# Kernel optimization log

Measured on AMD Instinct MI355X. Metric: run time of the kernel, lower is better.

The kernel has to match this reference:

```python
import jax, jax.numpy as jnp
import numpy as np

B, C, D = 16, 1024, 512
H = 8
E, K = 8, 2
FF = 4 * D
CAP_FACTOR = 1.25
T = B * C
CAP = int(CAP_FACTOR * T * K / E)  # 5120
EPS = 1e-5


def setup_inputs() -> dict:
    key = jax.random.key(0)
    ks = jax.random.split(key, 16)
    s = 0.02
    return {
        "x": jax.random.normal(ks[0], (B, C, D), jnp.float32),
        "src_mask": jnp.ones((B, 1, 1, C), jnp.int32),
        "wq": jax.random.normal(ks[1], (D, D), jnp.float32) * s,
        "bq": jnp.zeros((D,), jnp.float32),
        "wk": jax.random.normal(ks[2], (D, D), jnp.float32) * s,
        "bk": jnp.zeros((D,), jnp.float32),
        "wv": jax.random.normal(ks[3], (D, D), jnp.float32) * s,
        "bv": jnp.zeros((D,), jnp.float32),
        "wo": jax.random.normal(ks[4], (D, D), jnp.float32) * s,
        "bo": jnp.zeros((D,), jnp.float32),
        "ln1_g": jnp.ones((D,), jnp.float32),
        "ln1_b": jnp.zeros((D,), jnp.float32),
        "ln2_g": jnp.ones((D,), jnp.float32),
        "ln2_b": jnp.zeros((D,), jnp.float32),
        "router_w": jax.random.normal(ks[5], (D, E), jnp.float32) * s,
        "w1": jax.random.normal(ks[6], (E, D, FF), jnp.float32) * s,
        "b1": jnp.zeros((E, FF), jnp.float32),
        "w2": jax.random.normal(ks[7], (E, FF, D), jnp.float32) * s,
        "b2": jnp.zeros((E, D), jnp.float32),
    }


def _layernorm(z, g, b):
    m = z.mean(-1, keepdims=True)
    v = jnp.mean((z - m) ** 2, -1, keepdims=True)
    return (z - m) * jax.lax.rsqrt(v + EPS) * g + b


def _attention(x, mask, wq, bq, wk, bk, wv, bv, wo, bo):
    hd = D // H
    q = (x @ wq + bq).reshape(B, C, H, hd).transpose(0, 2, 1, 3)  # bhqd
    k = (x @ wk + bk).reshape(B, C, H, hd).transpose(0, 2, 1, 3)
    v = (x @ wv + bv).reshape(B, C, H, hd).transpose(0, 2, 1, 3)
    scores = jnp.einsum("bhqd,bhkd->bhqk", q, k) * (1.0 / np.sqrt(hd))
    scores = jnp.where(mask == 0, jnp.float32(-1e10), scores)
    attn = jax.nn.softmax(scores, axis=-1)
    o = jnp.einsum("bhqk,bhkd->bhqd", attn, v)
    o = o.transpose(0, 2, 1, 3).reshape(B, C, D)
    return o @ wo + bo


def _sparse_moe(x, router_w, w1, b1, w2, b2):
    xf = x.reshape(T, D)
    probs = jax.nn.softmax(xf @ router_w, axis=-1)  # [T, E]
    topv, topi = jax.lax.top_k(probs, K)            # [T, K]
    topv = topv / topv.sum(-1, keepdims=True)
    fe = topi.reshape(T * K)                        # expert id per slot
    oh = jax.nn.one_hot(fe, E, dtype=jnp.int32)     # [T*K, E]
    pos = (jnp.cumsum(oh, axis=0) * oh).sum(-1) - 1 # rank within expert
    keep = pos < CAP
    pos_safe = jnp.where(keep, pos, CAP)            # CAP -> dropped via mode='drop'
    tok = jnp.repeat(jnp.arange(T), K)
    disp = jnp.zeros((E, CAP, D), xf.dtype).at[fe, pos_safe].set(
        xf[tok], mode="drop")                       # [E, CAP, D]
    h = jax.nn.gelu(jnp.einsum("ecd,edf->ecf", disp, w1) + b1[:, None, :])
    y = jnp.einsum("ecf,efd->ecd", h, w2) + b2[:, None, :]
    gathered = y[fe, jnp.minimum(pos_safe, CAP - 1)]      # [T*K, D]
    gathered = jnp.where(keep[:, None], gathered, 0.0)
    out = (gathered.reshape(T, K, D) * topv[:, :, None]).sum(1)
    return out.reshape(B, C, D)


def reference(x, src_mask, wq, bq, wk, bk, wv, bv, wo, bo,
              ln1_g, ln1_b, ln2_g, ln2_b, router_w, w1, b1, w2, b2):
    attn_out = _attention(x, src_mask, wq, bq, wk, bk, wv, bv, wo, bo)
    src = _layernorm(x + attn_out, ln1_g, ln1_b)
    ff = _sparse_moe(src, router_w, w1, b1, w2, b2)
    return _layernorm(src + ff, ln2_g, ln2_b)
```

## Files before the change

### kernel.cpp

```cpp
#include <hip/hip_runtime.h>


#define DEV __device__ __forceinline__

typedef __bf16 bf16x8 __attribute__((ext_vector_type(8)));
typedef float  f32x4  __attribute__((ext_vector_type(4)));

typedef __attribute__((address_space(1))) unsigned char uchar_g;
typedef __attribute__((address_space(3))) unsigned char uchar_l;

DEV unsigned short f2bf(float f){
  __bf16 b = (__bf16)f;
  return __builtin_bit_cast(unsigned short, b);
}
DEV float bf2f(unsigned short h){
  return __builtin_bit_cast(float, ((unsigned)h) << 16);
}
DEV float geluf(float z){
  float a = 0.7978845608028654f*(z + 0.044715f*z*z*z);
  a = fminf(fmaxf(a, -15.f), 15.f);
  float u = __expf(-2.f*a);
  float th = (1.f - u) / (1.f + u);
  return 0.5f*z*(1.f + th);
}

template<int LOGROWB, int NBYTES>
DEV void stage_tile(char* lds, const char* g0, long stride, int tid){
  #pragma unroll
  for (int it = 0; it < NBYTES/4096; ++it){
    int o   = tid*16 + it*4096;
    int row = o >> LOGROWB;
    int b0  = o & ((1 << LOGROWB) - 1);
    int swz = (row & ((1 << (LOGROWB-4)) - 1)) << 4;
    const char* src = g0 + (long)row*stride + (b0 ^ swz);
    char* lb = lds + ((tid >> 6) << 10) + (it << 12);
    __builtin_amdgcn_global_load_lds((uchar_g*)src, (uchar_l*)lb, 16, 0, 0);
  }
}

DEV void stage_gather(char* lds, const char* base, const int* rowTok, int k0b, int tid){
  #pragma unroll
  for (int it = 0; it < 2; ++it){
    int o   = tid*16 + it*4096;
    int row = o >> 6;
    int b0  = o & 63;
    int swz = (row & 3) << 4;
    const char* src = base + (long)rowTok[row]*1024 + k0b + (b0 ^ swz);
    char* lb = lds + ((tid >> 6) << 10) + (it << 12);
    __builtin_amdgcn_global_load_lds((uchar_g*)src, (uchar_l*)lb, 16, 0, 0);
  }
}

template<int LOGROWB>
DEV bf16x8 frag(const char* lds, int row, int kByte){
  int swz = (row & ((1 << (LOGROWB-4)) - 1)) << 4;
  const char* p = lds + ((long)row << LOGROWB) + (kByte ^ swz);
  bf16x8 v;
  __builtin_memcpy(&v, __builtin_assume_aligned(p, 16), 16);
  return v;
}

DEV f32x4 mfma16(bf16x8 a, bf16x8 b, f32x4 c){
  return __builtin_amdgcn_mfma_f32_16x16x32_bf16(a, b, c, 0, 0, 0);
}

DEV float wsum64(float v){
  #pragma unroll
  for (int off = 32; off; off >>= 1) v += __shfl_xor(v, off);
  return v;
}
DEV float wsum16(float v){
  v += __shfl_xor(v, 1); v += __shfl_xor(v, 2);
  v += __shfl_xor(v, 4); v += __shfl_xor(v, 8);
  return v;
}
DEV float wmax16(float v){
  v = fmaxf(v, __shfl_xor(v, 1)); v = fmaxf(v, __shfl_xor(v, 2));
  v = fmaxf(v, __shfl_xor(v, 4)); v = fmaxf(v, __shfl_xor(v, 8));
  return v;
}


__global__ __launch_bounds__(256) void split_x_k(const float* __restrict__ x,
    unsigned short* __restrict__ xh, unsigned short* __restrict__ xl, int n4)
{
  int i = blockIdx.x*256 + threadIdx.x;
  if (i >= n4) return;
  float4 v = ((const float4*)x)[i];
  ushort4 h, lo;
  h.x = f2bf(v.x); lo.x = f2bf(v.x - bf2f(h.x));
  h.y = f2bf(v.y); lo.y = f2bf(v.y - bf2f(h.y));
  h.z = f2bf(v.z); lo.z = f2bf(v.z - bf2f(h.z));
  h.w = f2bf(v.w); lo.w = f2bf(v.w - bf2f(h.w));
  ((ushort4*)xh)[i] = h;
  ((ushort4*)xl)[i] = lo;
}

__global__ __launch_bounds__(256) void convT_k(const float* __restrict__ in,
    unsigned short* __restrict__ outh, unsigned short* __restrict__ outl,
    int K, int N, int rowOff)
{
  __shared__ float t[32][33];
  long zin  = (long)blockIdx.z * K * N;
  long zout = (long)blockIdx.z * N * K;
  int n0 = blockIdx.x*32, k0 = blockIdx.y*32;
  int cid = threadIdx.x & 31, rid = threadIdx.x >> 5;
  #pragma unroll
  for (int j = 0; j < 4; ++j){
    int r = rid + j*8;
    t[r][cid] = in[zin + (long)(k0+r)*N + n0 + cid];
  }
  __syncthreads();
  #pragma unroll
  for (int j = 0; j < 4; ++j){
    int nr = rid + j*8;
    float v = t[cid][nr];
    long o = zout + (long)(rowOff + n0 + nr)*K + k0 + cid;
    unsigned short hb = f2bf(v);
    outh[o] = hb;
    if (outl) outl[o] = f2bf(v - bf2f(hb));
  }
}

__global__ __launch_bounds__(256) void vtrans_k(const unsigned short* __restrict__ vin,
    unsigned short* __restrict__ vout)
{
  __shared__ unsigned short t[64][65];
  int bh = blockIdx.y, c0 = blockIdx.x*64;
  const unsigned short* src = vin + ((long)bh*1024 + c0)*64;
  for (int j = threadIdx.x; j < 4096; j += 256){
    int r = j >> 6, c = j & 63;
    t[r][c] = src[r*64 + c];
  }
  __syncthreads();
  unsigned short* dst = vout + (long)bh*64*1024 + c0;
  for (int j = threadIdx.x; j < 4096; j += 256){
    int d = j >> 6, cc = j & 63;
    dst[(long)d*1024 + cc] = t[cc][d];
  }
}


#define GEMM_PRE \
  const int tid = threadIdx.x, w = tid>>6, l = tid&63; \
  const int wm = (w>>1)*64, wn = (w&1)*64; \
  f32x4 acc[4][4] = {};

#define GEMM3_INNER(SAH,SAL,SBH,SBL) do { \
  const int kb = (l>>4)<<4; \
  bf16x8 ah_[4], al_[4], bh_[4], bl_[4]; \
  _Pragma("unroll") \
  for (int mt=0; mt<4; ++mt){ int r = wm+mt*16+(l&15); ah_[mt]=frag<6>(SAH,r,kb); al_[mt]=frag<6>(SAL,r,kb); } \
  _Pragma("unroll") \
  for (int nt=0; nt<4; ++nt){ int r = wn+nt*16+(l&15); bh_[nt]=frag<6>(SBH,r,kb); bl_[nt]=frag<6>(SBL,r,kb); } \
  _Pragma("unroll") \
  for (int mt=0; mt<4; ++mt) \
    _Pragma("unroll") \
    for (int nt=0; nt<4; ++nt){ \
      acc[mt][nt] = mfma16(ah_[mt], bh_[nt], acc[mt][nt]); \
      acc[mt][nt] = mfma16(ah_[mt], bl_[nt], acc[mt][nt]); \
      acc[mt][nt] = mfma16(al_[mt], bh_[nt], acc[mt][nt]); \
    } \
} while(0)

#define GEMM1_INNER(SA,SB) do { \
  const int kb = (l>>4)<<4; \
  bf16x8 a_[4], b_[4]; \
  _Pragma("unroll") \
  for (int mt=0; mt<4; ++mt){ a_[mt]=frag<6>(SA, wm+mt*16+(l&15), kb); } \
  _Pragma("unroll") \
  for (int nt=0; nt<4; ++nt){ b_[nt]=frag<6>(SB, wn+nt*16+(l&15), kb); } \
  _Pragma("unroll") \
  for (int mt=0; mt<4; ++mt) \
    _Pragma("unroll") \
    for (int nt=0; nt<4; ++nt) acc[mt][nt] = mfma16(a_[mt], b_[nt], acc[mt][nt]); \
} while(0)

__global__ __launch_bounds__(256) void gemm_qkv(
    const char* __restrict__ ah, const char* __restrict__ al,
    const char* __restrict__ bh, const char* __restrict__ bl,
    const float* __restrict__ bq, const float* __restrict__ bk, const float* __restrict__ bv,
    unsigned short* __restrict__ qh, unsigned short* __restrict__ ql,
    unsigned short* __restrict__ kh, unsigned short* __restrict__ kl,
    unsigned short* __restrict__ vh, unsigned short* __restrict__ vl)
{
  __shared__ __align__(16) char sAh[8192], sAl[8192], sBh[8192], sBl[8192];
  const int m0 = blockIdx.x*128, n0 = blockIdx.y*128;
  GEMM_PRE
  for (int k0 = 0; k0 < 512; k0 += 32){
    __syncthreads();
    stage_tile<6,8192>(sAh, ah + (long)m0*1024 + k0*2, 1024, tid);
    stage_tile<6,8192>(sAl, al + (long)m0*1024 + k0*2, 1024, tid);
    stage_tile<6,8192>(sBh, bh + (long)n0*1024 + k0*2, 1024, tid);
    stage_tile<6,8192>(sBl, bl + (long)n0*1024 + k0*2, 1024, tid);
    __syncthreads();
    GEMM3_INNER(sAh, sAl, sBh, sBl);
  }
  #pragma unroll
  for (int nt = 0; nt < 4; ++nt){
    int col = n0 + wn + nt*16 + (l&15);
    int mat = col >> 9;
    int dcol = col & 511;
    float bias = (mat==0) ? bq[dcol] : (mat==1) ? bk[dcol] : bv[dcol];
    unsigned short* dh = (mat==0) ? qh : (mat==1) ? kh : vh;
    unsigned short* dl = (mat==0) ? ql : (mat==1) ? kl : vl;
    int hh = dcol >> 6, dd = dcol & 63;
    #pragma unroll
    for (int mt = 0; mt < 4; ++mt)
      #pragma unroll
      for (int i = 0; i < 4; ++i){
        int rowg = m0 + wm + mt*16 + (l>>4)*4 + i;
        int b_ = rowg >> 10, c_ = rowg & 1023;
        long o = ((long)(b_*8 + hh)*1024 + c_)*64 + dd;
        float v = acc[mt][nt][i] + bias;
        unsigned short hb = f2bf(v);
        dh[o] = hb;
        dl[o] = f2bf(v - bf2f(hb));
      }
  }
}

__global__ __launch_bounds__(256) void gemm_oproj(
    const char* __restrict__ ah, const char* __restrict__ al,
    const char* __restrict__ bh, const char* __restrict__ bl,
    const float* __restrict__ bo, float* __restrict__ outp)
{
  __shared__ __align__(16) char sAh[8192], sAl[8192], sBh[8192], sBl[8192];
  const int m0 = blockIdx.x*128, n0 = blockIdx.y*128;
  GEMM_PRE
  for (int k0 = 0; k0 < 512; k0 += 32){
    __syncthreads();
    stage_tile<6,8192>(sAh, ah + (long)m0*1024 + k0*2, 1024, tid);
    stage_tile<6,8192>(sAl, al + (long)m0*1024 + k0*2, 1024, tid);
    stage_tile<6,8192>(sBh, bh + (long)n0*1024 + k0*2, 1024, tid);
    stage_tile<6,8192>(sBl, bl + (long)n0*1024 + k0*2, 1024, tid);
    __syncthreads();
    GEMM3_INNER(sAh, sAl, sBh, sBl);
  }
  #pragma unroll
  for (int nt = 0; nt < 4; ++nt){
    int col = n0 + wn + nt*16 + (l&15);
    float bias = bo[col];
    #pragma unroll
    for (int mt = 0; mt < 4; ++mt)
      #pragma unroll
      for (int i = 0; i < 4; ++i){
        int rowg = m0 + wm + mt*16 + (l>>4)*4 + i;
        outp[(long)rowg*512 + col] = acc[mt][nt][i] + bias;
      }
  }
}

__global__ __launch_bounds__(256) void gemm_ffn1(
    const char* __restrict__ srcb, const int* __restrict__ idx, const int* __restrict__ cntc,
    const char* __restrict__ w1T, const float* __restrict__ b1,
    unsigned short* __restrict__ hbuf, int ffc, int rr)
{
  const int e = blockIdx.z;
  const int m0 = blockIdx.x*128;
  if (m0 >= cntc[e]) return;
  const int n0 = blockIdx.y*128;
  const int ffg0 = rr*ffc;
  __shared__ __align__(16) char sA[8192], sB[8192];
  GEMM_PRE
  for (int k0 = 0; k0 < 512; k0 += 32){
    __syncthreads();
    stage_gather(sA, srcb, idx + e*5120 + m0, k0*2, tid);
    stage_tile<6,8192>(sB, w1T + ((long)e*2048 + ffg0 + n0)*1024 + k0*2, 1024, tid);
    __syncthreads();
    GEMM1_INNER(sA, sB);
  }
  #pragma unroll
  for (int nt = 0; nt < 4; ++nt){
    int colc = n0 + wn + nt*16 + (l&15);
    float bias = b1[e*2048 + ffg0 + colc];
    #pragma unroll
    for (int mt = 0; mt < 4; ++mt)
      #pragma unroll
      for (int i = 0; i < 4; ++i){
        int rowg = m0 + wm + mt*16 + (l>>4)*4 + i;
        float v = geluf(acc[mt][nt][i] + bias);
        hbuf[((long)e*5120 + rowg)*ffc + colc] = f2bf(v);
      }
  }
}

__global__ __launch_bounds__(256) void gemm_ffn2(
    const unsigned short* __restrict__ hbuf, const int* __restrict__ cntc,
    const char* __restrict__ w2T, const float* __restrict__ b2,
    float* __restrict__ y, int ffc, int rr)
{
  const int e = blockIdx.z;
  const int m0 = blockIdx.x*128;
  if (m0 >= cntc[e]) return;
  const int n0 = blockIdx.y*128;
  __shared__ __align__(16) char sA[8192], sB[8192];
  GEMM_PRE
  for (int k0 = 0; k0 < ffc; k0 += 32){
    __syncthreads();
    stage_tile<6,8192>(sA, (const char*)hbuf + ((long)e*5120 + m0)*(ffc*2) + k0*2, ffc*2, tid);
    stage_tile<6,8192>(sB, w2T + ((long)e*512 + n0)*4096 + (rr*ffc + k0)*2, 4096, tid);
    __syncthreads();
    GEMM1_INNER(sA, sB);
  }
  #pragma unroll
  for (int nt = 0; nt < 4; ++nt){
    int col = n0 + wn + nt*16 + (l&15);
    #pragma unroll
    for (int mt = 0; mt < 4; ++mt)
      #pragma unroll
      for (int i = 0; i < 4; ++i){
        int rowg = m0 + wm + mt*16 + (l>>4)*4 + i;
        long o = ((long)e*5120 + rowg)*512 + col;
        float base = (rr == 0) ? b2[e*512 + col] : y[o];
        y[o] = base + acc[mt][nt][i];
      }
  }
}

__global__ __launch_bounds__(256) void flash_attn(
    const char* __restrict__ qh, const char* __restrict__ ql,
    const char* __restrict__ kh, const char* __restrict__ kl,
    const char* __restrict__ vth, const char* __restrict__ vtl,
    const int* __restrict__ msk,
    unsigned short* __restrict__ oh, unsigned short* __restrict__ ol)
{
  __shared__ __align__(16) char lds[49152];
  char* sKh = lds;
  char* sKl = lds + 8192;
  char* sVh = lds + 16384;
  char* sVl = lds + 24576;
  const int tid = threadIdx.x, w = tid>>6, l = tid&63;
  const int q0 = blockIdx.x*64;
  const int bh = blockIdx.y, b_ = bh>>3, h_ = bh&7;
  char* pw = lds + 32768 + w*4096;

  stage_tile<7,8192>(lds,        qh + ((long)bh*1024 + q0)*128, 128, tid);
  stage_tile<7,8192>(lds + 8192, ql + ((long)bh*1024 + q0)*128, 128, tid);
  __syncthreads();
  bf16x8 qfh[2], qfl[2];
  const int ra = w*16 + (l&15);
  #pragma unroll
  for (int ks = 0; ks < 2; ++ks){
    const int kb = ks*64 + ((l>>4)<<4);
    qfh[ks] = frag<7>(lds,        ra, kb);
    qfl[ks] = frag<7>(lds + 8192, ra, kb);
  }

  float mrow[4], lrow[4];
  f32x4 oacc[4] = {};
  #pragma unroll
  for (int i = 0; i < 4; ++i){ mrow[i] = -1e30f; lrow[i] = 0.0f; }
  const int* mb = msk + b_*1024;

  for (int kv0 = 0; kv0 < 1024; kv0 += 64){
    __syncthreads();
    stage_tile<7,8192>(sKh, kh + ((long)bh*1024 + kv0)*128, 128, tid);
    stage_tile<7,8192>(sKl, kl + ((long)bh*1024 + kv0)*128, 128, tid);
    stage_tile<7,8192>(sVh, vth + (long)bh*131072 + kv0*2, 2048, tid);
    stage_tile<7,8192>(sVl, vtl + (long)bh*131072 + kv0*2, 2048, tid);
    __syncthreads();

    f32x4 sacc[4] = {};
    __builtin_amdgcn_s_setprio(1);
    #pragma unroll
    for (int ks = 0; ks < 2; ++ks){
      const int kb = ks*64 + ((l>>4)<<4);
      #pragma unroll
      for (int nt = 0; nt < 4; ++nt){
        const int rb = nt*16 + (l&15);
        bf16x8 b_h = frag<7>(sKh, rb, kb);
        bf16x8 b_l = frag<7>(sKl, rb, kb);
        sacc[nt] = mfma16(qfh[ks], b_h, sacc[nt]);
        sacc[nt] = mfma16(qfh[ks], b_l, sacc[nt]);
        sacc[nt] = mfma16(qfl[ks], b_h, sacc[nt]);
      }
    }
    __builtin_amdgcn_s_setprio(0);

    float sv[4][4];
    #pragma unroll
    for (int nt = 0; nt < 4; ++nt){
      int mk = mb[kv0 + nt*16 + (l&15)];
      #pragma unroll
      for (int i = 0; i < 4; ++i){
        float s = sacc[nt][i] * 0.125f;
        sv[nt][i] = (mk == 0) ? -1e10f : s;
      }
    }
    float tmax[4]; bool need = false;
    #pragma unroll
    for (int i = 0; i < 4; ++i){
      float tm = fmaxf(fmaxf(sv[0][i], sv[1][i]), fmaxf(sv[2][i], sv[3][i]));
      tmax[i] = wmax16(tm);
      need |= (tmax[i] > mrow[i] + 8.0f);
    }
    if (__ballot(need) != 0ull){
      #pragma unroll
      for (int i = 0; i < 4; ++i){
        float mn  = fmaxf(mrow[i], tmax[i]);
        float fsc = __expf(mrow[i] - mn);
        lrow[i] *= fsc; mrow[i] = mn;
        #pragma unroll
        for (int dt = 0; dt < 4; ++dt) oacc[dt][i] *= fsc;
      }
    }
    float tsum[4] = {0,0,0,0};
    float pf[4][4];
    #pragma unroll
    for (int nt = 0; nt < 4; ++nt)
      #pragma unroll
      for (int i = 0; i < 4; ++i){
        float p = __expf(sv[nt][i] - mrow[i]);
        pf[nt][i] = p; tsum[i] += p;
      }
    #pragma unroll
    for (int i = 0; i < 4; ++i) lrow[i] += wsum16(tsum[i]);

    #pragma unroll
    for (int nt = 0; nt < 4; ++nt)
      #pragma unroll
      for (int i = 0; i < 4; ++i){
        int r = (l>>4)*4 + i;
        int cbyte = (nt*16 + (l&15))*2;
        int off = r*128 + (cbyte ^ ((r&7)<<4));
        unsigned short hb = f2bf(pf[nt][i]);
        *(unsigned short*)(pw + off)        = hb;
        *(unsigned short*)(pw + 2048 + off) = f2bf(pf[nt][i] - bf2f(hb));
      }
    __builtin_amdgcn_s_setprio(1);
    #pragma unroll
    for (int ks = 0; ks < 2; ++ks){
      const int kb = ks*64 + ((l>>4)<<4);
      bf16x8 p_h = frag<7>(pw,        l&15, kb);
      bf16x8 p_l = frag<7>(pw + 2048, l&15, kb);
      #pragma unroll
      for (int dt = 0; dt < 4; ++dt){
        const int rv = dt*16 + (l&15);
        bf16x8 v_h = frag<7>(sVh, rv, kb);
        bf16x8 v_l = frag<7>(sVl, rv, kb);
        oacc[dt] = mfma16(p_h, v_h, oacc[dt]);
        oacc[dt] = mfma16(p_h, v_l, oacc[dt]);
        oacc[dt] = mfma16(p_l, v_h, oacc[dt]);
      }
    }
    __builtin_amdgcn_s_setprio(0);
  }
  #pragma unroll
  for (int dt = 0; dt < 4; ++dt)
    #pragma unroll
    for (int i = 0; i < 4; ++i){
      float val = oacc[dt][i] / lrow[i];
      int qg = q0 + w*16 + (l>>4)*4 + i;
      long o = ((long)(b_*1024 + qg))*512 + h_*64 + dt*16 + (l&15);
      unsigned short hb = f2bf(val);
      oh[o] = hb;
      ol[o] = f2bf(val - bf2f(hb));
    }
}


__global__ __launch_bounds__(256) void ln1_k(const float* __restrict__ x,
    const float* __restrict__ attn, const float* __restrict__ g, const float* __restrict__ bb,
    float* __restrict__ src, unsigned short* __restrict__ srcb)
{
  const int w = threadIdx.x >> 6, l = threadIdx.x & 63;
  const long t = (long)blockIdx.x*4 + w;
  const float* xr = x + t*512;
  const float* ar = attn + t*512;
  float z[8]; float s = 0.f;
  #pragma unroll
  for (int j = 0; j < 8; ++j){ int d = l + j*64; z[j] = xr[d] + ar[d]; s += z[j]; }
  s = wsum64(s);
  float mean = s * (1.f/512.f);
  float vs = 0.f;
  #pragma unroll
  for (int j = 0; j < 8; ++j){ float d = z[j]-mean; vs += d*d; }
  vs = wsum64(vs);
  float rstd = 1.f / sqrtf(vs*(1.f/512.f) + 1e-5f);
  #pragma unroll
  for (int j = 0; j < 8; ++j){
    int d = l + j*64;
    float o = (z[j]-mean)*rstd*g[d] + bb[d];
    src[t*512 + d] = o;
    srcb[t*512 + d] = f2bf(o);
  }
}

__global__ __launch_bounds__(256) void router_k(const float* __restrict__ src,
    const float* __restrict__ rw, int* __restrict__ topi, float* __restrict__ topv)
{
  const int w = threadIdx.x >> 6, l = threadIdx.x & 63;
  const long t = (long)blockIdx.x*4 + w;
  const float* xr = src + t*512;
  float acc[8] = {0,0,0,0,0,0,0,0};
  #pragma unroll
  for (int j = 0; j < 8; ++j){
    int d = l + j*64;
    float xv = xr[d];
    #pragma unroll
    for (int e = 0; e < 8; ++e) acc[e] += xv * rw[d*8 + e];
  }
  #pragma unroll
  for (int e = 0; e < 8; ++e) acc[e] = wsum64(acc[e]);
  int i1 = 0; float v1 = acc[0];
  #pragma unroll
  for (int e = 1; e < 8; ++e){ if (acc[e] > v1){ v1 = acc[e]; i1 = e; } }
  int i2 = -1; float v2 = -1e30f;
  #pragma unroll
  for (int e = 0; e < 8; ++e){ if (e != i1 && acc[e] > v2){ v2 = acc[e]; i2 = e; } }
  if (l == 0){
    topi[2*t]   = i1;
    topi[2*t+1] = i2;
    topv[2*t]   = 1.0f / (1.0f + __expf(v2 - v1));
    topv[2*t+1] = 1.0f / (1.0f + __expf(v1 - v2));
  }
}

__global__ __launch_bounds__(1024) void rank_k(const int* __restrict__ topi,
    int* __restrict__ pos, int* __restrict__ idx, int* __restrict__ cntc)
{
  __shared__ int hist[1024][8];
  const int t = threadIdx.x;
  for (int j = t; j < 8*5120; j += 1024) idx[j] = 0;
  int c[8] = {0,0,0,0,0,0,0,0};
  const int base = t*32;
  for (int j = 0; j < 32; ++j){
    int e = topi[base + j];
    #pragma unroll
    for (int e2 = 0; e2 < 8; ++e2) c[e2] += (e == e2);
  }
  #pragma unroll
  for (int e2 = 0; e2 < 8; ++e2) hist[t][e2] = c[e2];
  __syncthreads();
  const int wv = t >> 6, l = t & 63;
  if (wv < 8){
    int vals[16]; int s = 0;
    #pragma unroll
    for (int j = 0; j < 16; ++j){ vals[j] = hist[l*16 + j][wv]; s += vals[j]; }
    int sc = s;
    #pragma unroll
    for (int off = 1; off < 64; off <<= 1){
      int n = __shfl_up(sc, off);
      if (l >= off) sc += n;
    }
    int run = sc - s;
    #pragma unroll
    for (int j = 0; j < 16; ++j){ int v = vals[j]; hist[l*16 + j][wv] = run; run += v; }
    if (l == 63) cntc[wv] = (run < 5120) ? run : 5120;
  }
  __syncthreads();
  int r2[8];
  #pragma unroll
  for (int e2 = 0; e2 < 8; ++e2) r2[e2] = hist[t][e2];
  for (int j = 0; j < 32; ++j){
    int slot = base + j;
    int e = topi[slot];
    int p = 0;
    #pragma unroll
    for (int e2 = 0; e2 < 8; ++e2){ int m = (e == e2); p += m ? r2[e2] : 0; r2[e2] += m; }
    pos[slot] = p;
    if (p < 5120) idx[e*5120 + p] = slot >> 1;
  }
}

__global__ __launch_bounds__(256) void final_k(const float* __restrict__ src,
    const float* __restrict__ y, const int* __restrict__ topi,
    const float* __restrict__ topv, const int* __restrict__ pos,
    const float* __restrict__ g, const float* __restrict__ bb,
    float* __restrict__ out)
{
  const int w = threadIdx.x >> 6, l = threadIdx.x & 63;
  const long t = (long)blockIdx.x*4 + w;
  const int e0 = topi[2*t], e1 = topi[2*t+1];
  const int p0 = pos[2*t],  p1 = pos[2*t+1];
  const float w0 = topv[2*t], w1 = topv[2*t+1];
  const bool k0 = (p0 < 5120), k1 = (p1 < 5120);
  const float* y0 = y + ((long)e0*5120 + (k0 ? p0 : 0))*512;
  const float* y1 = y + ((long)e1*5120 + (k1 ? p1 : 0))*512;
  const float* sr = src + t*512;
  float z[8]; float s = 0.f;
  #pragma unroll
  for (int j = 0; j < 8; ++j){
    int d = l + j*64;
    float f0 = k0 ? y0[d] : 0.f;
    float f1 = k1 ? y1[d] : 0.f;
    z[j] = sr[d] + w0*f0 + w1*f1;
    s += z[j];
  }
  s = wsum64(s);
  float mean = s * (1.f/512.f);
  float vs = 0.f;
  #pragma unroll
  for (int j = 0; j < 8; ++j){ float d = z[j]-mean; vs += d*d; }
  vs = wsum64(vs);
  float rstd = 1.f / sqrtf(vs*(1.f/512.f) + 1e-5f);
  #pragma unroll
  for (int j = 0; j < 8; ++j){
    int d = l + j*64;
    out[t*512 + d] = (z[j]-mean)*rstd*g[d] + bb[d];
  }
}


extern "C" void kernel_launch(void* const* d_in, const int* in_sizes, int n_in,
                              void* d_out, int out_size, void* d_ws, size_t ws_size,
                              hipStream_t stream)
{
  const float* x   = (const float*)d_in[0];
  const int*   msk = (const int*)  d_in[1];
  const float* wq  = (const float*)d_in[2];
  const float* bq  = (const float*)d_in[3];
  const float* wk  = (const float*)d_in[4];
  const float* bk  = (const float*)d_in[5];
  const float* wv  = (const float*)d_in[6];
  const float* bv  = (const float*)d_in[7];
  const float* wo  = (const float*)d_in[8];
  const float* bo  = (const float*)d_in[9];
  const float* g1  = (const float*)d_in[10];
  const float* be1 = (const float*)d_in[11];
  const float* g2  = (const float*)d_in[12];
  const float* be2 = (const float*)d_in[13];
  const float* rw  = (const float*)d_in[14];
  const float* w1  = (const float*)d_in[15];
  const float* b1  = (const float*)d_in[16];
  const float* w2  = (const float*)d_in[17];
  const float* b2  = (const float*)d_in[18];
  float* out = (float*)d_out;
  char* ws = (char*)d_ws;

  const long SZ = 16777216;
  char* xh = ws;             char* xl = ws + SZ;
  char* oh = xh;             char* ol = xl;
  char* qh = ws + 2*SZ;      char* ql = ws + 3*SZ;
  float* oproj = (float*)(ws + 2*SZ);
  char* vth = ws + 4*SZ;     char* vtl = ws + 5*SZ;
  float* ybuf = (float*)ws;
  char* kh = ws + 6*SZ;      char* kl = ws + 7*SZ;
  float* srcf = (float*)(ws + 6*SZ);
  char* vh = ws + 8*SZ;      char* vl = ws + 9*SZ;
  char* srcb = ws + 8*SZ;
  int*   topi  = (int*)  (ws + 9*SZ);
  float* topv  = (float*)(ws + 9*SZ + 131072);
  int*   pos   = (int*)  (ws + 9*SZ + 262144);
  int*   idx   = (int*)  (ws + 9*SZ + 393216);
  int*   cntc  = (int*)  (ws + 9*SZ + 557056);
  char* wqkvTh = ws + 10*SZ;
  char* wqkvTl = wqkvTh + 1572864;
  char* woTh   = wqkvTl + 1572864;
  char* woTl   = woTh + 524288;
  char* w1T    = woTl + 524288;
  char* w2T    = w1T + SZ;
  char* hbuf   = w2T + SZ;

  int R = 8;
  {
    size_t base = (size_t)(hbuf - ws);
    const int cand[4] = {1, 2, 4, 8};
    for (int i = 0; i < 4; ++i){
      size_t need = base + (size_t)167772160 / (size_t)cand[i];
      if (need <= ws_size){ R = cand[i]; break; }
    }
  }
  const int FFC = 2048 / R;

  split_x_k<<<8192,256,0,stream>>>(x, (unsigned short*)xh, (unsigned short*)xl, 2097152);
  convT_k<<<dim3(16,16,1),256,0,stream>>>(wq, (unsigned short*)wqkvTh, (unsigned short*)wqkvTl, 512, 512, 0);
  convT_k<<<dim3(16,16,1),256,0,stream>>>(wk, (unsigned short*)wqkvTh, (unsigned short*)wqkvTl, 512, 512, 512);
  convT_k<<<dim3(16,16,1),256,0,stream>>>(wv, (unsigned short*)wqkvTh, (unsigned short*)wqkvTl, 512, 512, 1024);
  convT_k<<<dim3(16,16,1),256,0,stream>>>(wo, (unsigned short*)woTh, (unsigned short*)woTl, 512, 512, 0);
  convT_k<<<dim3(64,16,8),256,0,stream>>>(w1, (unsigned short*)w1T, nullptr, 512, 2048, 0);
  convT_k<<<dim3(16,64,8),256,0,stream>>>(w2, (unsigned short*)w2T, nullptr, 2048, 512, 0);

  gemm_qkv<<<dim3(128,12),256,0,stream>>>(xh, xl, wqkvTh, wqkvTl, bq, bk, bv,
      (unsigned short*)qh, (unsigned short*)ql, (unsigned short*)kh, (unsigned short*)kl,
      (unsigned short*)vh, (unsigned short*)vl);
  vtrans_k<<<dim3(16,128),256,0,stream>>>((const unsigned short*)vh, (unsigned short*)vth);
  vtrans_k<<<dim3(16,128),256,0,stream>>>((const unsigned short*)vl, (unsigned short*)vtl);
  flash_attn<<<dim3(16,128),256,0,stream>>>(qh, ql, kh, kl, vth, vtl, msk,
      (unsigned short*)oh, (unsigned short*)ol);
  gemm_oproj<<<dim3(128,4),256,0,stream>>>(oh, ol, woTh, woTl, bo, oproj);
  ln1_k<<<4096,256,0,stream>>>(x, oproj, g1, be1, srcf, (unsigned short*)srcb);

  router_k<<<4096,256,0,stream>>>(srcf, rw, topi, topv);
  rank_k<<<1,1024,0,stream>>>(topi, pos, idx, cntc);

  for (int rr = 0; rr < R; ++rr){
    gemm_ffn1<<<dim3(40, FFC/128, 8),256,0,stream>>>(srcb, idx, cntc, w1T, b1,
        (unsigned short*)hbuf, FFC, rr);
    gemm_ffn2<<<dim3(40, 4, 8),256,0,stream>>>((const unsigned short*)hbuf, cntc, w2T, b2,
        ybuf, FFC, rr);
  }

  final_k<<<4096,256,0,stream>>>(srcf, ybuf, topi, topv, pos, g2, be2, out);
}
```

Baseline: 928.2 us.

## Chunk MoE FFN by expert groups instead of FF slices; fuse LN1 with router

The MoE FFN loop is now split over groups of experts instead of slices of the hidden FF dimension. Each ffn2 launch therefore runs the full K=2048 reduction and writes y once with the bias, instead of reading y back and accumulating across rounds. LayerNorm1 and the router are merged into one kernel so the normalized activations are not written and then read again. Flash attention now multiplies by a reciprocal of the row sum instead of dividing. The cost is fewer blocks per launch when R>1, which may lower occupancy.

Result: faster. 843.5 us (-9.1%).

```diff
diff --git a/kernel.cpp b/kernel.cpp
--- a/kernel.cpp
+++ b/kernel.cpp
@@ -254,66 +254,67 @@
 __global__ __launch_bounds__(256) void gemm_ffn1(
     const char* __restrict__ srcb, const int* __restrict__ idx, const int* __restrict__ cntc,
     const char* __restrict__ w1T, const float* __restrict__ b1,
-    unsigned short* __restrict__ hbuf, int ffc, int rr)
-{
-  const int e = blockIdx.z;
-  const int m0 = blockIdx.x*128;
-  if (m0 >= cntc[e]) return;
-  const int n0 = blockIdx.y*128;
-  const int ffg0 = rr*ffc;
-  __shared__ __align__(16) char sA[8192], sB[8192];
-  GEMM_PRE
-  for (int k0 = 0; k0 < 512; k0 += 32){
-    __syncthreads();
-    stage_gather(sA, srcb, idx + e*5120 + m0, k0*2, tid);
-    stage_tile<6,8192>(sB, w1T + ((long)e*2048 + ffg0 + n0)*1024 + k0*2, 1024, tid);
-    __syncthreads();
-    GEMM1_INNER(sA, sB);
-  }
-  #pragma unroll
-  for (int nt = 0; nt < 4; ++nt){
-    int colc = n0 + wn + nt*16 + (l&15);
-    float bias = b1[e*2048 + ffg0 + colc];
-    #pragma unroll
-    for (int mt = 0; mt < 4; ++mt)
-      #pragma unroll
-      for (int i = 0; i < 4; ++i){
-        int rowg = m0 + wm + mt*16 + (l>>4)*4 + i;
-        float v = geluf(acc[mt][nt][i] + bias);
-        hbuf[((long)e*5120 + rowg)*ffc + colc] = f2bf(v);
-      }
-  }
-}
-
-__global__ __launch_bounds__(256) void gemm_ffn2(
-    const unsigned short* __restrict__ hbuf, const int* __restrict__ cntc,
-    const char* __restrict__ w2T, const float* __restrict__ b2,
-    float* __restrict__ y, int ffc, int rr)
-{
-  const int e = blockIdx.z;
+    unsigned short* __restrict__ hbuf, int eg0)
+{
+  const int zl = blockIdx.z;
+  const int e = eg0 + zl;
   const int m0 = blockIdx.x*128;
   if (m0 >= cntc[e]) return;
   const int n0 = blockIdx.y*128;
   __shared__ __align__(16) char sA[8192], sB[8192];
   GEMM_PRE
-  for (int k0 = 0; k0 < ffc; k0 += 32){
-    __syncthreads();
-    stage_tile<6,8192>(sA, (const char*)hbuf + ((long)e*5120 + m0)*(ffc*2) + k0*2, ffc*2, tid);
-    stage_tile<6,8192>(sB, w2T + ((long)e*512 + n0)*4096 + (rr*ffc + k0)*2, 4096, tid);
+  for (int k0 = 0; k0 < 512; k0 += 32){
+    __syncthreads();
+    stage_gather(sA, srcb, idx + e*5120 + m0, k0*2, tid);
+    stage_tile<6,8192>(sB, w1T + ((long)e*2048 + n0)*1024 + k0*2, 1024, tid);
+    __syncthreads();
+    GEMM1_INNER(sA, sB);
+  }
+  #pragma unroll
+  for (int nt = 0; nt < 4; ++nt){
+    int colc = n0 + wn + nt*16 + (l&15);
+    float bias = b1[e*2048 + colc];
+    #pragma unroll
+    for (int mt = 0; mt < 4; ++mt)
+      #pragma unroll
+      for (int i = 0; i < 4; ++i){
+        int rowg = m0 + wm + mt*16 + (l>>4)*4 + i;
+        float v = geluf(acc[mt][nt][i] + bias);
+        hbuf[((long)zl*5120 + rowg)*2048 + colc] = f2bf(v);
+      }
+  }
+}
+
+__global__ __launch_bounds__(256) void gemm_ffn2(
+    const unsigned short* __restrict__ hbuf, const int* __restrict__ cntc,
+    const char* __restrict__ w2T, const float* __restrict__ b2,
+    float* __restrict__ y, int eg0)
+{
+  const int zl = blockIdx.z;
+  const int e = eg0 + zl;
+  const int m0 = blockIdx.x*128;
+  if (m0 >= cntc[e]) return;
+  const int n0 = blockIdx.y*128;
+  __shared__ __align__(16) char sA[8192], sB[8192];
+  GEMM_PRE
+  for (int k0 = 0; k0 < 2048; k0 += 32){
+    __syncthreads();
+    stage_tile<6,8192>(sA, (const char*)hbuf + ((long)zl*5120 + m0)*4096 + k0*2, 4096, tid);
+    stage_tile<6,8192>(sB, w2T + ((long)e*512 + n0)*4096 + k0*2, 4096, tid);
     __syncthreads();
     GEMM1_INNER(sA, sB);
   }
   #pragma unroll
   for (int nt = 0; nt < 4; ++nt){
     int col = n0 + wn + nt*16 + (l&15);
+    float bias = b2[e*512 + col];
     #pragma unroll
     for (int mt = 0; mt < 4; ++mt)
       #pragma unroll
       for (int i = 0; i < 4; ++i){
         int rowg = m0 + wm + mt*16 + (l>>4)*4 + i;
         long o = ((long)e*5120 + rowg)*512 + col;
-        float base = (rr == 0) ? b2[e*512 + col] : y[o];
-        y[o] = base + acc[mt][nt][i];
+        y[o] = bias + acc[mt][nt][i];
       }
   }
 }
@@ -446,11 +447,14 @@
     }
     __builtin_amdgcn_s_setprio(0);
   }
+  float rli[4];
+  #pragma unroll
+  for (int i = 0; i < 4; ++i) rli[i] = 1.0f / lrow[i];
   #pragma unroll
   for (int dt = 0; dt < 4; ++dt)
     #pragma unroll
     for (int i = 0; i < 4; ++i){
-      float val = oacc[dt][i] / lrow[i];
+      float val = oacc[dt][i] * rli[i];
       int qg = q0 + w*16 + (l>>4)*4 + i;
       long o = ((long)(b_*1024 + qg))*512 + h_*64 + dt*16 + (l&15);
       unsigned short hb = f2bf(val);
@@ -460,9 +464,11 @@
 }
 
 
-__global__ __launch_bounds__(256) void ln1_k(const float* __restrict__ x,
+__global__ __launch_bounds__(256) void ln1_router_k(const float* __restrict__ x,
     const float* __restrict__ attn, const float* __restrict__ g, const float* __restrict__ bb,
-    float* __restrict__ src, unsigned short* __restrict__ srcb)
+    const float* __restrict__ rw,
+    float* __restrict__ src, unsigned short* __restrict__ srcb,
+    int* __restrict__ topi, float* __restrict__ topv)
 {
   const int w = threadIdx.x >> 6, l = threadIdx.x & 63;
   const long t = (long)blockIdx.x*4 + w;
@@ -478,38 +484,25 @@
   for (int j = 0; j < 8; ++j){ float d = z[j]-mean; vs += d*d; }
   vs = wsum64(vs);
   float rstd = 1.f / sqrtf(vs*(1.f/512.f) + 1e-5f);
+  float racc[8] = {0,0,0,0,0,0,0,0};
   #pragma unroll
   for (int j = 0; j < 8; ++j){
     int d = l + j*64;
     float o = (z[j]-mean)*rstd*g[d] + bb[d];
     src[t*512 + d] = o;
     srcb[t*512 + d] = f2bf(o);
-  }
-}
-
-__global__ __launch_bounds__(256) void router_k(const float* __restrict__ src,
-    const float* __restrict__ rw, int* __restrict__ topi, float* __restrict__ topv)
-{
-  const int w = threadIdx.x >> 6, l = threadIdx.x & 63;
-  const long t = (long)blockIdx.x*4 + w;
-  const float* xr = src + t*512;
-  float acc[8] = {0,0,0,0,0,0,0,0};
-  #pragma unroll
-  for (int j = 0; j < 8; ++j){
-    int d = l + j*64;
-    float xv = xr[d];
-    #pragma unroll
-    for (int e = 0; e < 8; ++e) acc[e] += xv * rw[d*8 + e];
-  }
-  #pragma unroll
-  for (int e = 0; e < 8; ++e) acc[e] = wsum64(acc[e]);
-  int i1 = 0; float v1 = acc[0];
-  #pragma unroll
-  for (int e = 1; e < 8; ++e){ if (acc[e] > v1){ v1 = acc[e]; i1 = e; } }
-  int i2 = -1; float v2 = -1e30f;
-  #pragma unroll
-  for (int e = 0; e < 8; ++e){ if (e != i1 && acc[e] > v2){ v2 = acc[e]; i2 = e; } }
+    #pragma unroll
+    for (int e = 0; e < 8; ++e) racc[e] += o * rw[d*8 + e];
+  }
+  #pragma unroll
+  for (int e = 0; e < 8; ++e) racc[e] = wsum64(racc[e]);
   if (l == 0){
+    int i1 = 0; float v1 = racc[0];
+    #pragma unroll
+    for (int e = 1; e < 8; ++e){ if (racc[e] > v1){ v1 = racc[e]; i1 = e; } }
+    int i2 = -1; float v2 = -1e30f;
+    #pragma unroll
+    for (int e = 0; e < 8; ++e){ if (e != i1 && racc[e] > v2){ v2 = racc[e]; i2 = e; } }
     topi[2*t]   = i1;
     topi[2*t+1] = i2;
     topv[2*t]   = 1.0f / (1.0f + __expf(v2 - v1));
@@ -662,7 +655,7 @@
       if (need <= ws_size){ R = cand[i]; break; }
     }
   }
-  const int FFC = 2048 / R;
+  const int EG = 8 / R;
 
   split_x_k<<<8192,256,0,stream>>>(x, (unsigned short*)xh, (unsigned short*)xl, 2097152);
   convT_k<<<dim3(16,16,1),256,0,stream>>>(wq, (unsigned short*)wqkvTh, (unsigned short*)wqkvTl, 512, 512, 0);
@@ -680,16 +673,16 @@
   flash_attn<<<dim3(16,128),256,0,stream>>>(qh, ql, kh, kl, vth, vtl, msk,
       (unsigned short*)oh, (unsigned short*)ol);
   gemm_oproj<<<dim3(128,4),256,0,stream>>>(oh, ol, woTh, woTl, bo, oproj);
-  ln1_k<<<4096,256,0,stream>>>(x, oproj, g1, be1, srcf, (unsigned short*)srcb);
-
-  router_k<<<4096,256,0,stream>>>(srcf, rw, topi, topv);
+  ln1_router_k<<<4096,256,0,stream>>>(x, oproj, g1, be1, rw, srcf,
+      (unsigned short*)srcb, topi, topv);
+
   rank_k<<<1,1024,0,stream>>>(topi, pos, idx, cntc);
 
-  for (int rr = 0; rr < R; ++rr){
-    gemm_ffn1<<<dim3(40, FFC/128, 8),256,0,stream>>>(srcb, idx, cntc, w1T, b1,
-        (unsigned short*)hbuf, FFC, rr);
-    gemm_ffn2<<<dim3(40, 4, 8),256,0,stream>>>((const unsigned short*)hbuf, cntc, w2T, b2,
-        ybuf, FFC, rr);
+  for (int g = 0; g < R; ++g){
+    gemm_ffn1<<<dim3(40, 16, EG),256,0,stream>>>(srcb, idx, cntc, w1T, b1,
+        (unsigned short*)hbuf, g*EG);
+    gemm_ffn2<<<dim3(40, 4, EG),256,0,stream>>>((const unsigned short*)hbuf, cntc, w2T, b2,
+        ybuf, g*EG);
   }
 
   final_k<<<4096,256,0,stream>>>(srcf, ybuf, topi, topv, pos, g2, be2, out);
```
